# Optimization experiments

Measured on AMD Instinct MI355X. Metric: run time of the kernel, lower is better.

The kernel has to match this reference:

```python
import jax, jax.numpy as jnp
import numpy as np

D_MODEL = 512
NHEAD = 8
HEAD_DIM = D_MODEL // NHEAD  # 64
ROTARY_DIM = HEAD_DIM        # rotary_dim defaults to head_dim
WINDOW = (127, 128)          # (left, right) sliding window, flash-attn convention
ROPE_BASE = 10000.0


def setup_inputs() -> dict:
    key = jax.random.key(0)
    k1, k2, k3, k4 = jax.random.split(key, 4)
    N, T = 4, 2048
    x = jax.random.normal(k1, (N, T, D_MODEL), dtype=jnp.float32)
    # Wqkv: Linear(d_model, 3*d_model, bias=False) -> weight [3*D, D]
    Wqkv_w = jax.random.normal(k2, (3 * D_MODEL, D_MODEL), dtype=jnp.float32) * (D_MODEL ** -0.5)
    # out_proj: Linear(d_model, d_model, bias=True)
    out_w = jax.random.normal(k3, (D_MODEL, D_MODEL), dtype=jnp.float32) * (D_MODEL ** -0.5)
    out_b = jax.random.normal(k4, (D_MODEL,), dtype=jnp.float32) * 0.01
    return {"x": x, "Wqkv_w": Wqkv_w, "out_w": out_w, "out_b": out_b}


def _rope_cos_sin(T, dtype):
    # flash-attn RotaryEmbedding: inv_freq over even indices of rotary_dim
    inv_freq = 1.0 / (ROPE_BASE ** (jnp.arange(0, ROTARY_DIM, 2, dtype=jnp.float32) / ROTARY_DIM))
    t = jnp.arange(T, dtype=jnp.float32)
    freqs = jnp.outer(t, inv_freq)  # [T, ROTARY_DIM//2]
    return jnp.cos(freqs).astype(dtype), jnp.sin(freqs).astype(dtype)


def _apply_rotary(x, cos, sin):
    # non-interleaved (rotate halves); x: [N, T, H, hd], rotary over first ROTARY_DIM dims
    r, rest = x[..., :ROTARY_DIM], x[..., ROTARY_DIM:]
    half = ROTARY_DIM // 2
    x1, x2 = r[..., :half], r[..., half:]
    c = cos[None, :, None, :]  # [1, T, 1, half]
    s = sin[None, :, None, :]
    rotated = jnp.concatenate([x1 * c - x2 * s, x2 * c + x1 * s], axis=-1)
    return jnp.concatenate([rotated, rest], axis=-1) if rest.shape[-1] else rotated


def reference(x, Wqkv_w, out_w, out_b):
    N, T, D = x.shape
    qkv = jnp.einsum('ntd,ed->nte', x, Wqkv_w).reshape(N, T, 3, NHEAD, HEAD_DIM)
    q, k, v = qkv[:, :, 0], qkv[:, :, 1], qkv[:, :, 2]  # each [N, T, H, hd]
    cos, sin = _rope_cos_sin(T, x.dtype)
    q = _apply_rotary(q, cos, sin)
    k = _apply_rotary(k, cos, sin)
    scale = HEAD_DIM ** -0.5
    scores = jnp.einsum('nthd,nshd->nhts', q, k) * scale  # [N, H, T, T]
    # sliding window: query i attends key j iff i - left <= j <= i + right
    i = jnp.arange(T)[:, None]
    j = jnp.arange(T)[None, :]
    mask = (j >= i - WINDOW[0]) & (j <= i + WINDOW[1])  # [T, T]
    scores = jnp.where(mask[None, None], scores, jnp.finfo(scores.dtype).min)
    attn = jax.nn.softmax(scores, axis=-1)
    ctx = jnp.einsum('nhts,nshd->nthd', attn, v).reshape(N, T, D)
    return jnp.einsum('ntd,ed->nte', ctx, out_w) + out_b
```

## Files before the change

### kernel.cpp

```cpp
#include <hip/hip_runtime.h>
#include <math.h>

#define TSEQ 2048
#define NB 4
#define DM 512
#define NH 8
#define HD 64

typedef _Float16 half8 __attribute__((ext_vector_type(8)));
typedef _Float16 half4 __attribute__((ext_vector_type(4)));
typedef float floatx4 __attribute__((ext_vector_type(4)));

#if __has_builtin(__builtin_amdgcn_exp2f)
#define EXP2F(x) __builtin_amdgcn_exp2f(x)
#else
#define EXP2F(x) exp2f(x)
#endif

__device__ __forceinline__ void gl2lds16(const _Float16* g, _Float16* l) {
  const __attribute__((address_space(1))) unsigned int* gp =
      (const __attribute__((address_space(1))) unsigned int*)(uintptr_t)g;
  __attribute__((address_space(3))) unsigned int* lp =
      (__attribute__((address_space(3))) unsigned int*)(uintptr_t)l;
  __builtin_amdgcn_global_load_lds(gp, lp, 16, 0, 0);
}


#define WS_END_U16 2916352

__global__ void prep(const float* __restrict__ x, const float* __restrict__ wqkv,
                     const float* __restrict__ ow, char* __restrict__ ws) {
  for (int i = blockIdx.x * 256 + threadIdx.x; i < WS_END_U16; i += 2048 * 256) {
    if (i < 524288) {
      const float4 a = ((const float4*)x)[2 * i];
      const float4 b = ((const float4*)x)[2 * i + 1];
      half8 h;
      h[0] = (_Float16)a.x; h[1] = (_Float16)a.y; h[2] = (_Float16)a.z; h[3] = (_Float16)a.w;
      h[4] = (_Float16)b.x; h[5] = (_Float16)b.y; h[6] = (_Float16)b.z; h[7] = (_Float16)b.w;
      *(half8*)(ws + (size_t)i * 16) = h;
    } else if (i >= 540672 && i < 638976) {
      const int o = i - 540672;
      const float4 a = ((const float4*)wqkv)[2 * o];
      const float4 b = ((const float4*)wqkv)[2 * o + 1];
      half8 h;
      h[0] = (_Float16)a.x; h[1] = (_Float16)a.y; h[2] = (_Float16)a.z; h[3] = (_Float16)a.w;
      h[4] = (_Float16)b.x; h[5] = (_Float16)b.y; h[6] = (_Float16)b.z; h[7] = (_Float16)b.w;
      *(half8*)(ws + (size_t)i * 16) = h;
    } else if (i >= 655360 && i < 688128) {
      const int o = i - 655360;
      const float4 a = ((const float4*)ow)[2 * o];
      const float4 b = ((const float4*)ow)[2 * o + 1];
      half8 h;
      h[0] = (_Float16)a.x; h[1] = (_Float16)a.y; h[2] = (_Float16)a.z; h[3] = (_Float16)a.w;
      h[4] = (_Float16)b.x; h[5] = (_Float16)b.y; h[6] = (_Float16)b.z; h[7] = (_Float16)b.w;
      *(half8*)(ws + (size_t)i * 16) = h;
    } else if (i >= 2883584) {
      const int u = i - 2883584;
      float4 o4;
      {
        const int id = 2 * u, t = id >> 5, fi = id & 31;
        const float invf = powf(10000.0f, -(float)(2 * fi) * (1.0f / 64.0f));
        float s, c; sincosf((float)t * invf, &s, &c);
        o4.x = c; o4.y = s;
      }
      {
        const int id = 2 * u + 1, t = id >> 5, fi = id & 31;
        const float invf = powf(10000.0f, -(float)(2 * fi) * (1.0f / 64.0f));
        float s, c; sincosf((float)t * invf, &s, &c);
        o4.z = c; o4.w = s;
      }
      ((float4*)(ws + 46137344))[u] = o4;
    } else {
      ((float4*)ws)[i] = make_float4(0.f, 0.f, 0.f, 0.f);
    }
  }
}

__global__ __launch_bounds__(256) void qkv_gemm_mfma(
    const _Float16* __restrict__ A, const _Float16* __restrict__ B,
    const float2* __restrict__ rope,
    _Float16* __restrict__ qb, _Float16* __restrict__ kb, _Float16* __restrict__ vT)
{
  __shared__ __align__(16) _Float16 As[128 * 32];
  __shared__ __align__(16) _Float16 Bs[128 * 32];
  const int tid = threadIdx.x;
  const int wv = tid >> 6, lane = tid & 63, quad = lane >> 4, col = lane & 15;
  const int wm = wv >> 1, we = wv & 1;
  const int m0 = blockIdx.x << 7, c0 = blockIdx.y << 7;
  const int r0 = tid >> 2, p0 = tid & 3;
  const int cA0 = (p0 - (r0 >> 1)) & 3;
  const int r1 = (tid + 256) >> 2, p1 = tid & 3;
  const int cA1 = (p1 - (r1 >> 1)) & 3;
  const _Float16* ga0 = &A[(size_t)(m0 + r0) * DM + cA0 * 8];
  const _Float16* ga1 = &A[(size_t)(m0 + r1) * DM + cA1 * 8];
  const _Float16* gb0 = &B[(size_t)(c0 + r0) * DM + cA0 * 8];
  const _Float16* gb1 = &B[(size_t)(c0 + r1) * DM + cA1 * 8];
  _Float16* la0 = &As[tid * 8];
  _Float16* la1 = &As[(tid + 256) * 8];
  _Float16* lb0 = &Bs[tid * 8];
  _Float16* lb1 = &Bs[(tid + 256) * 8];
  floatx4 acc[4][4] = {};
  for (int k0 = 0; k0 < DM; k0 += 32) {
    __syncthreads();
    gl2lds16(ga0 + k0, la0);
    gl2lds16(ga1 + k0, la1);
    gl2lds16(gb0 + k0, lb0);
    gl2lds16(gb1 + k0, lb1);
    __syncthreads();
    half8 af[4], bf[4];
#pragma unroll
    for (int mt = 0; mt < 4; mt++) {
      const int R = wm * 64 + mt * 16 + col;
      af[mt] = *(const half8*)&As[R * 32 + (((quad + (R >> 1)) & 3) << 3)];
    }
#pragma unroll
    for (int et = 0; et < 4; et++) {
      const int R = we * 64 + et * 16 + col;
      bf[et] = *(const half8*)&Bs[R * 32 + (((quad + (R >> 1)) & 3) << 3)];
    }
#pragma unroll
    for (int mt = 0; mt < 4; mt++)
#pragma unroll
      for (int et = 0; et < 4; et++)
        acc[mt][et] = __builtin_amdgcn_mfma_f32_16x16x32_f16(af[mt], bf[et], acc[mt][et], 0, 0, 0);
  }
  const int eidx = (c0 >> 6) + we;
  const int three = eidx >> 3, h = eidx & 7;
  const int mbase = m0 + wm * 64 + quad * 4;
  if (three == 2) {
#pragma unroll
    for (int mt = 0; mt < 4; mt++) {
      const int m = mbase + mt * 16;
      const int n = m >> 11, t = m & 2047;
#pragma unroll
      for (int et = 0; et < 4; et++) {
        const int dh = et * 16 + col;
        half4 hv;
#pragma unroll
        for (int r = 0; r < 4; r++) hv[r] = (_Float16)acc[mt][et][r];
        *(half4*)&vT[(size_t)(n * NH + h) * HD * TSEQ + (size_t)dh * TSEQ + t] = hv;
      }
    }
  } else {
    _Float16* dst = three ? kb : qb;
    const float scl = three ? 1.0f : 0.125f * 1.4426950408889634f;
#pragma unroll
    for (int mt = 0; mt < 4; mt++)
#pragma unroll
      for (int r = 0; r < 4; r++) {
        const int m = mbase + mt * 16 + r;
        const int n = m >> 11, t = m & 2047;
#pragma unroll
        for (int et = 0; et < 4; et++) {
          const int i = ((et & 1) << 4) + col;
          const float2 cs = rope[t * 32 + i];
          const float v = acc[mt][et][r];
          const float v2 = acc[mt][et ^ 2][r];
          const float o = (et < 2) ? (v * cs.x - v2 * cs.y) : (v * cs.x + v2 * cs.y);
          dst[((size_t)(n * NH + h) * TSEQ + t) * HD + et * 16 + col] = (_Float16)(o * scl);
        }
      }
  }
}

__global__ __launch_bounds__(256, 4) void attn_win_mfma(
    const _Float16* __restrict__ qb, const _Float16* __restrict__ kb,
    const _Float16* __restrict__ vT, _Float16* __restrict__ ctx)
{
  __shared__ __align__(16) char smem[36864];
  _Float16* Ks = (_Float16*)smem;
  _Float16* Vt = (_Float16*)(smem + 9216);
  _Float16* Ps = (_Float16*)(smem + 18432);
  _Float16* Osh = (_Float16*)(smem + 27648);

  const int tid = threadIdx.x;
  const int wv = tid >> 6;
  const int lane = tid & 63;
  const int quad = lane >> 4;
  const int col = lane & 15;
  const int nh = blockIdx.y;
  const int q0 = blockIdx.x << 6;
  const _Float16* qp = qb + (size_t)nh * TSEQ * HD;
  const _Float16* kp = kb + (size_t)nh * TSEQ * HD;
  const _Float16* vp = vT + (size_t)nh * HD * TSEQ;

  const int i_row = (wv << 4) + col;
  const int ig = q0 + i_row;
  const half8 qf0 = *(const half8*)&qp[(size_t)ig * HD + (quad << 3)];
  const half8 qf1 = *(const half8*)&qp[(size_t)ig * HD + 32 + (quad << 3)];

  float l_i = 0.0f;
  floatx4 accO[4] = {};

  const int kt0 = max(0, q0 - 127) >> 6;
  const int kt1 = min(TSEQ - 1, q0 + 191) >> 6;
  const int kr = tid >> 2, kc = (tid & 3) << 4;
  const int vd = tid >> 2, vc = (tid & 3) << 4;
  for (int kt = kt0; kt <= kt1; kt++) {
    const int j0 = kt << 6;
    const half8 k0_ = *(const half8*)&kp[(size_t)(j0 + kr) * HD + kc];
    const half8 k1_ = *(const half8*)&kp[(size_t)(j0 + kr) * HD + kc + 8];
    const half8 v0_ = *(const half8*)&vp[(size_t)vd * TSEQ + j0 + vc];
    const half8 v1_ = *(const half8*)&vp[(size_t)vd * TSEQ + j0 + vc + 8];
    __syncthreads();
    *(half8*)&Ks[kr * 72 + kc] = k0_;
    *(half8*)&Ks[kr * 72 + kc + 8] = k1_;
    *(half8*)&Vt[vd * 72 + vc] = v0_;
    *(half8*)&Vt[vd * 72 + vc + 8] = v1_;
    __syncthreads();

    floatx4 S[4];
#pragma unroll
    for (int js = 0; js < 4; js++) {
      const half8 a0 = *(const half8*)&Ks[((js << 4) + col) * 72 + (quad << 3)];
      const half8 a1 = *(const half8*)&Ks[((js << 4) + col) * 72 + 32 + (quad << 3)];
      floatx4 c = {0.f, 0.f, 0.f, 0.f};
      c = __builtin_amdgcn_mfma_f32_16x16x32_f16(a0, qf0, c, 0, 0, 0);
      c = __builtin_amdgcn_mfma_f32_16x16x32_f16(a1, qf1, c, 0, 0, 0);
      S[js] = c;
    }
#pragma unroll
    for (int js = 0; js < 4; js++) {
      half4 ph;
#pragma unroll
      for (int r = 0; r < 4; r++) {
        const int jg = j0 + (js << 4) + (quad << 2) + r;
        const bool valid = (jg >= ig - 127) && (jg <= ig + 128);
        const float p = valid ? EXP2F(S[js][r]) : 0.0f;
        l_i += p;
        ph[r] = (_Float16)p;
      }
      *(half4*)&Ps[i_row * 72 + (js << 4) + (quad << 2)] = ph;
    }
    const half8 pa0 = *(const half8*)&Ps[i_row * 72 + (quad << 3)];
    const half8 pa1 = *(const half8*)&Ps[i_row * 72 + 32 + (quad << 3)];
#pragma unroll
    for (int d4 = 0; d4 < 4; d4++) {
      const half8 vb0 = *(const half8*)&Vt[((d4 << 4) + col) * 72 + (quad << 3)];
      const half8 vb1 = *(const half8*)&Vt[((d4 << 4) + col) * 72 + 32 + (quad << 3)];
      accO[d4] = __builtin_amdgcn_mfma_f32_16x16x32_f16(pa0, vb0, accO[d4], 0, 0, 0);
      accO[d4] = __builtin_amdgcn_mfma_f32_16x16x32_f16(pa1, vb1, accO[d4], 0, 0, 0);
    }
  }
  l_i += __shfl_xor(l_i, 16, 64);
  l_i += __shfl_xor(l_i, 32, 64);
  {
    const float linv = 1.0f / l_i;
    float l4[4];
#pragma unroll
    for (int r = 0; r < 4; r++) l4[r] = __shfl(linv, (quad << 2) + r, 64);
#pragma unroll
    for (int d4 = 0; d4 < 4; d4++)
#pragma unroll
      for (int r = 0; r < 4; r++)
        Osh[((wv << 4) + (quad << 2) + r) * 72 + (d4 << 4) + col] = (_Float16)(accO[d4][r] * l4[r]);
  }
  __syncthreads();
  {
    const int n = nh >> 3, h = nh & 7;
    const int oi = tid >> 2, oc = (tid & 3) << 4;
    _Float16* dst = &ctx[((size_t)n * TSEQ + q0 + oi) * DM + h * HD + oc];
    *(half8*)&dst[0] = *(const half8*)&Osh[oi * 72 + oc];
    *(half8*)&dst[8] = *(const half8*)&Osh[oi * 72 + oc + 8];
  }
}

__global__ __launch_bounds__(256) void out_gemm_mfma(
    const _Float16* __restrict__ A, const _Float16* __restrict__ B,
    const float* __restrict__ bias, float* __restrict__ out)
{
  __shared__ _Float16 As[128 * 40];
  __shared__ _Float16 Bs[64 * 40];
  const int tid = threadIdx.x;
  const int wv = tid >> 6, lane = tid & 63, quad = lane >> 4, col = lane & 15;
  const int wm = wv >> 1, we = wv & 1;
  const int m0 = blockIdx.x << 7, c0 = blockIdx.y << 6;
  const int sr = tid >> 1, sc = (tid & 1) << 4;
  const int br = tid >> 2, bc = (tid & 3) << 3;
  const _Float16* ap = &A[(size_t)(m0 + sr) * DM + sc];
  const _Float16* bp = &B[(size_t)(c0 + br) * DM + bc];
  floatx4 acc[4][2] = {};
  for (int k0 = 0; k0 < DM; k0 += 32) {
    const half8 a0 = *(const half8*)(ap + k0);
    const half8 a1 = *(const half8*)(ap + k0 + 8);
    const half8 b0 = *(const half8*)(bp + k0);
    __syncthreads();
    *(half8*)&As[sr * 40 + sc] = a0;
    *(half8*)&As[sr * 40 + sc + 8] = a1;
    *(half8*)&Bs[br * 40 + bc] = b0;
    __syncthreads();
    half8 af[4], bf[2];
#pragma unroll
    for (int mt = 0; mt < 4; mt++)
      af[mt] = *(const half8*)&As[(wm * 64 + mt * 16 + col) * 40 + quad * 8];
#pragma unroll
    for (int et = 0; et < 2; et++)
      bf[et] = *(const half8*)&Bs[(we * 32 + et * 16 + col) * 40 + quad * 8];
#pragma unroll
    for (int mt = 0; mt < 4; mt++)
#pragma unroll
      for (int et = 0; et < 2; et++)
        acc[mt][et] = __builtin_amdgcn_mfma_f32_16x16x32_f16(af[mt], bf[et], acc[mt][et], 0, 0, 0);
  }
  float bb[2];
#pragma unroll
  for (int et = 0; et < 2; et++) bb[et] = bias[c0 + we * 32 + et * 16 + col];
  const int mbase = m0 + wm * 64 + quad * 4;
#pragma unroll
  for (int mt = 0; mt < 4; mt++)
#pragma unroll
    for (int r = 0; r < 4; r++) {
      const int m = mbase + mt * 16 + r;
#pragma unroll
      for (int et = 0; et < 2; et++)
        out[(size_t)m * DM + c0 + we * 32 + et * 16 + col] = acc[mt][et][r] + bb[et];
    }
}

extern "C" void kernel_launch(void* const* d_in, const int* in_sizes, int n_in,
                              void* d_out, int out_size, void* d_ws, size_t ws_size,
                              hipStream_t stream) {
  const float* x    = (const float*)d_in[0];
  const float* wqkv = (const float*)d_in[1];
  const float* ow   = (const float*)d_in[2];
  const float* ob   = (const float*)d_in[3];
  char* ws = (char*)d_ws;
  _Float16* xh    = (_Float16*)(ws);
  _Float16* wqkvh = (_Float16*)(ws + 8650752);
  _Float16* owh   = (_Float16*)(ws + 10485760);
  _Float16* qbuf  = (_Float16*)(ws + 11534336);
  _Float16* kbuf  = (_Float16*)(ws + 20971520);
  _Float16* vTb   = (_Float16*)(ws + 29360128);
  _Float16* ctxh  = (_Float16*)(ws + 37748736);
  float2*   rope  = (float2*)  (ws + 46137344);

  prep<<<2048, 256, 0, stream>>>(x, wqkv, ow, ws);
  qkv_gemm_mfma<<<dim3(64, 12), 256, 0, stream>>>(xh, wqkvh, rope, qbuf, kbuf, vTb);
  attn_win_mfma<<<dim3(32, 32), 256, 0, stream>>>(qbuf, kbuf, vTb, ctxh);
  out_gemm_mfma<<<dim3(64, 8), 256, 0, stream>>>(ctxh, owh, ob, (float*)d_out);
}
```

Baseline: 135.5 us.

## Drop workspace zero-fill in prep, prefetch K/V tiles into registers

The prep kernel no longer zero-fills the whole workspace. It now launches one thread per conversion or rope unit, removing tens of megabytes of store traffic plus the grid-stride loop. The attention kernel loads the next K/V tile from global memory into registers while the current tile is being computed, so load latency overlaps with MFMA work. The sliding-window mask test becomes a single unsigned range compare. The risk is that some later kernel relied on zeroed padding regions, and that the prefetch registers lower occupancy.

```diff
diff --git a/kernel.cpp b/kernel.cpp
--- a/kernel.cpp
+++ b/kernel.cpp
@@ -26,53 +26,43 @@
 }
 
 
-#define WS_END_U16 2916352
+__device__ __forceinline__ void cvt8(const float* __restrict__ src, char* __restrict__ dst,
+                                     int unit_src, int unit_dst) {
+  const float4 a = ((const float4*)src)[2 * unit_src];
+  const float4 b = ((const float4*)src)[2 * unit_src + 1];
+  half8 h;
+  h[0] = (_Float16)a.x; h[1] = (_Float16)a.y; h[2] = (_Float16)a.z; h[3] = (_Float16)a.w;
+  h[4] = (_Float16)b.x; h[5] = (_Float16)b.y; h[6] = (_Float16)b.z; h[7] = (_Float16)b.w;
+  *(half8*)(dst + (size_t)unit_dst * 16) = h;
+}
 
 __global__ void prep(const float* __restrict__ x, const float* __restrict__ wqkv,
                      const float* __restrict__ ow, char* __restrict__ ws) {
-  for (int i = blockIdx.x * 256 + threadIdx.x; i < WS_END_U16; i += 2048 * 256) {
-    if (i < 524288) {
-      const float4 a = ((const float4*)x)[2 * i];
-      const float4 b = ((const float4*)x)[2 * i + 1];
-      half8 h;
-      h[0] = (_Float16)a.x; h[1] = (_Float16)a.y; h[2] = (_Float16)a.z; h[3] = (_Float16)a.w;
-      h[4] = (_Float16)b.x; h[5] = (_Float16)b.y; h[6] = (_Float16)b.z; h[7] = (_Float16)b.w;
-      *(half8*)(ws + (size_t)i * 16) = h;
-    } else if (i >= 540672 && i < 638976) {
-      const int o = i - 540672;
-      const float4 a = ((const float4*)wqkv)[2 * o];
-      const float4 b = ((const float4*)wqkv)[2 * o + 1];
-      half8 h;
-      h[0] = (_Float16)a.x; h[1] = (_Float16)a.y; h[2] = (_Float16)a.z; h[3] = (_Float16)a.w;
-      h[4] = (_Float16)b.x; h[5] = (_Float16)b.y; h[6] = (_Float16)b.z; h[7] = (_Float16)b.w;
-      *(half8*)(ws + (size_t)i * 16) = h;
-    } else if (i >= 655360 && i < 688128) {
-      const int o = i - 655360;
-      const float4 a = ((const float4*)ow)[2 * o];
-      const float4 b = ((const float4*)ow)[2 * o + 1];
-      half8 h;
-      h[0] = (_Float16)a.x; h[1] = (_Float16)a.y; h[2] = (_Float16)a.z; h[3] = (_Float16)a.w;
-      h[4] = (_Float16)b.x; h[5] = (_Float16)b.y; h[6] = (_Float16)b.z; h[7] = (_Float16)b.w;
-      *(half8*)(ws + (size_t)i * 16) = h;
-    } else if (i >= 2883584) {
-      const int u = i - 2883584;
-      float4 o4;
-      {
-        const int id = 2 * u, t = id >> 5, fi = id & 31;
-        const float invf = powf(10000.0f, -(float)(2 * fi) * (1.0f / 64.0f));
-        float s, c; sincosf((float)t * invf, &s, &c);
-        o4.x = c; o4.y = s;
-      }
-      {
-        const int id = 2 * u + 1, t = id >> 5, fi = id & 31;
-        const float invf = powf(10000.0f, -(float)(2 * fi) * (1.0f / 64.0f));
-        float s, c; sincosf((float)t * invf, &s, &c);
-        o4.z = c; o4.w = s;
-      }
-      ((float4*)(ws + 46137344))[u] = o4;
-    } else {
-      ((float4*)ws)[i] = make_float4(0.f, 0.f, 0.f, 0.f);
-    }
+  const int i = blockIdx.x * 256 + threadIdx.x;
+  if (i < 524288) {
+    cvt8(x, ws, i, i);
+  } else if (i < 622592) {
+    const int o = i - 524288;
+    cvt8(wqkv, ws + 8650752, o, o);
+  } else if (i < 655360) {
+    const int o = i - 622592;
+    cvt8(ow, ws + 10485760, o, o);
+  } else {
+    const int u = i - 655360;
+    float4 o4;
+    {
+      const int id = 2 * u, t = id >> 5, fi = id & 31;
+      const float invf = powf(10000.0f, -(float)(2 * fi) * (1.0f / 64.0f));
+      float s, c; sincosf((float)t * invf, &s, &c);
+      o4.x = c; o4.y = s;
+    }
+    {
+      const int id = 2 * u + 1, t = id >> 5, fi = id & 31;
+      const float invf = powf(10000.0f, -(float)(2 * fi) * (1.0f / 64.0f));
+      float s, c; sincosf((float)t * invf, &s, &c);
+      o4.z = c; o4.w = s;
+    }
+    ((float4*)(ws + 46137344))[u] = o4;
   }
 }
 
@@ -196,18 +186,30 @@
   const int kt1 = min(TSEQ - 1, q0 + 191) >> 6;
   const int kr = tid >> 2, kc = (tid & 3) << 4;
   const int vd = tid >> 2, vc = (tid & 3) << 4;
+  const _Float16* kpr = kp + (size_t)kr * HD + kc;
+  const _Float16* vpr = vp + (size_t)vd * TSEQ + vc;
+
+  half8 ck0 = *(const half8*)(kpr + (size_t)(kt0 << 6) * HD);
+  half8 ck1 = *(const half8*)(kpr + (size_t)(kt0 << 6) * HD + 8);
+  half8 cv0 = *(const half8*)(vpr + (kt0 << 6));
+  half8 cv1 = *(const half8*)(vpr + (kt0 << 6) + 8);
+
   for (int kt = kt0; kt <= kt1; kt++) {
     const int j0 = kt << 6;
-    const half8 k0_ = *(const half8*)&kp[(size_t)(j0 + kr) * HD + kc];
-    const half8 k1_ = *(const half8*)&kp[(size_t)(j0 + kr) * HD + kc + 8];
-    const half8 v0_ = *(const half8*)&vp[(size_t)vd * TSEQ + j0 + vc];
-    const half8 v1_ = *(const half8*)&vp[(size_t)vd * TSEQ + j0 + vc + 8];
-    __syncthreads();
-    *(half8*)&Ks[kr * 72 + kc] = k0_;
-    *(half8*)&Ks[kr * 72 + kc + 8] = k1_;
-    *(half8*)&Vt[vd * 72 + vc] = v0_;
-    *(half8*)&Vt[vd * 72 + vc + 8] = v1_;
-    __syncthreads();
+    __syncthreads();
+    *(half8*)&Ks[kr * 72 + kc] = ck0;
+    *(half8*)&Ks[kr * 72 + kc + 8] = ck1;
+    *(half8*)&Vt[vd * 72 + vc] = cv0;
+    *(half8*)&Vt[vd * 72 + vc + 8] = cv1;
+    __syncthreads();
+
+    {
+      const int jn = (kt < kt1) ? (j0 + 64) : j0;
+      ck0 = *(const half8*)(kpr + (size_t)jn * HD);
+      ck1 = *(const half8*)(kpr + (size_t)jn * HD + 8);
+      cv0 = *(const half8*)(vpr + jn);
+      cv1 = *(const half8*)(vpr + jn + 8);
+    }
 
     floatx4 S[4];
 #pragma unroll
@@ -219,13 +221,13 @@
       c = __builtin_amdgcn_mfma_f32_16x16x32_f16(a1, qf1, c, 0, 0, 0);
       S[js] = c;
     }
+    const int relb = j0 - ig + 127 + (quad << 2);
 #pragma unroll
     for (int js = 0; js < 4; js++) {
       half4 ph;
 #pragma unroll
       for (int r = 0; r < 4; r++) {
-        const int jg = j0 + (js << 4) + (quad << 2) + r;
-        const bool valid = (jg >= ig - 127) && (jg <= ig + 128);
+        const bool valid = (unsigned)(relb + (js << 4) + r) < 256u;
         const float p = valid ? EXP2F(S[js][r]) : 0.0f;
         l_i += p;
         ph[r] = (_Float16)p;
@@ -334,7 +336,7 @@
   _Float16* ctxh  = (_Float16*)(ws + 37748736);
   float2*   rope  = (float2*)  (ws + 46137344);
 
-  prep<<<2048, 256, 0, stream>>>(x, wqkv, ow, ws);
+  prep<<<2688, 256, 0, stream>>>(x, wqkv, ow, ws);
   qkv_gemm_mfma<<<dim3(64, 12), 256, 0, stream>>>(xh, wqkvh, rope, qbuf, kbuf, vTb);
   attn_win_mfma<<<dim3(32, 32), 256, 0, stream>>>(qbuf, kbuf, vTb, ctxh);
   out_gemm_mfma<<<dim3(64, 8), 256, 0, stream>>>(ctxh, owh, ob, (float*)d_out);
```

Result: faster. 130.4 us (-3.8%).
